# Optimization experiments

Measured on AMD Instinct MI355X. Metric: run time of the kernel, lower is better.

The kernel has to match this reference:

```python
import jax, jax.numpy as jnp
import numpy as np

FORWARD_WEIGHT = 1.0  # ChamferLoss(forward_weight=1.0)


def _chamfer_dists(pred, gt):
    """Bidirectional squared NN distances.
    pred: (B,N,3), gt: (B,M,3) -> dist1 (B,N), dist2 (B,M).
    Uses ||x-y||^2 = ||x||^2 + ||y||^2 - 2<x,y> to avoid the (B,N,M,3) diff tensor.
    """
    xx = jnp.sum(pred * pred, axis=-1)                 # (B,N)
    yy = jnp.sum(gt * gt, axis=-1)                     # (B,M)
    xy = jnp.einsum('bnd,bmd->bnm', pred, gt)          # (B,N,M)
    d = xx[:, :, None] + yy[:, None, :] - 2.0 * xy     # (B,N,M) squared distances
    dist1 = jnp.min(d, axis=2)                         # pred -> gt, (B,N)
    dist2 = jnp.min(d, axis=1)                         # gt -> pred, (B,M)
    return dist1, dist2


def setup_inputs() -> dict:
    key = jax.random.key(0)
    k1, k2 = jax.random.split(key)
    B, N, M = 4, 8192, 8192
    pred = jax.random.normal(k1, (B, N, 3), dtype=jnp.float32)
    gt = jax.random.normal(k2, (B, M, 3), dtype=jnp.float32)
    return {"pred": pred, "gt": gt}


def reference(pred, gt):
    # ChamferLoss.forward with defaults: no threshold, no masks, percentage=1.0,
    # forward_weight=1.0, reduction='mean'.
    dist1, dist2 = _chamfer_dists(pred, gt)
    pred2gt = jnp.mean(dist1, axis=1)                  # (B,)
    gt2pred = jnp.mean(dist2, axis=1)                  # (B,)
    cd_dist = FORWARD_WEIGHT * pred2gt + gt2pred
    return jnp.mean(cd_dist)
```

## Files before the change

kernel.cpp:

```cpp
#include <hip/hip_runtime.h>

typedef short short8 __attribute__((ext_vector_type(8)));
typedef float floatx16 __attribute__((ext_vector_type(16)));

#define B_    4
#define NPTS  8192
#define IS    16
#define JS    16
#define ITB   512
#define JTB   512
#define NT    4
#define NJT   16
#define TOT   (B_ * NPTS)

#define A0OFF 0
#define A1OFF 516
#define B0OFF 1032
#define B1OFF 1548
#define LDS8N 2060


__device__ __forceinline__ unsigned short bf16h(float v) {
  unsigned u = __float_as_uint(v);
  return (unsigned short)((u + 0x7FFFu + ((u >> 16) & 1u)) >> 16);
}
__device__ __forceinline__ void bf16split(float v, unsigned short& h, unsigned short& l) {
  h = bf16h(v);
  l = bf16h(v - __uint_as_float((unsigned)h << 16));
}

__device__ __forceinline__ void pack_dst(const float* g, short8& s0, short8& s1) {
  const float x = g[0], y = g[1], z = g[2];
  const float w = fmaf(x, x, fmaf(y, y, z * z));
  unsigned short xh, xl, yh, yl, zh, zl, wh, wl;
  bf16split(-2.f * x, xh, xl); bf16split(-2.f * y, yh, yl);
  bf16split(-2.f * z, zh, zl); bf16split(w, wh, wl);
  s0 = (short8){(short)xh,(short)xh,(short)xl,(short)xl,
                (short)yh,(short)yh,(short)yl,(short)yl};
  s1 = (short8){(short)zh,(short)zh,(short)zl,(short)zl,
                (short)wh,(short)wl,(short)0x3F80,(short)0x3F80};
}
__device__ __forceinline__ void pack_src(const float* p, short8& s0, short8& s1) {
  const float x = p[0], y = p[1], z = p[2];
  const float qq = fmaf(x, x, fmaf(y, y, z * z));
  unsigned short xh, xl, yh, yl, zh, zl, qh, ql;
  bf16split(x, xh, xl); bf16split(y, yh, yl);
  bf16split(z, zh, zl); bf16split(qq, qh, ql);
  s0 = (short8){(short)xh,(short)xl,(short)xh,(short)xl,
                (short)yh,(short)yl,(short)yh,(short)yl};
  s1 = (short8){(short)zh,(short)zl,(short)zh,(short)zl,
                (short)0x3F80,(short)0x3F80,(short)qh,(short)ql};
}

__global__ __launch_bounds__(256, 4) void mfma_pass_kernel(
    const float* __restrict__ pred, const float* __restrict__ gt,
    unsigned* __restrict__ slots) {
  __shared__ short8 lds8[LDS8N];

  const int zb  = blockIdx.z;
  const int dir = zb >> 2;
  const int b   = zb & 3;
  const float* src = dir ? gt   : pred;
  const float* dst = dir ? pred : gt;

  const int tid   = threadIdx.x;
  const int lane  = tid & 63;
  const int w     = tid >> 6;
  const int jbase = blockIdx.y * JTB;
  const int ibase = blockIdx.x * ITB;

#pragma unroll
  for (int r = 0; r < 2; ++r) {
    const int pt = tid + r * 256;
    short8 s0, s1;
    pack_dst(dst + ((size_t)b * NPTS + jbase + pt) * 3, s0, s1);
    lds8[A0OFF + pt] = s0;
    lds8[A1OFF + pt] = s1;
    pack_src(src + ((size_t)b * NPTS + ibase + pt) * 3, s0, s1);
    lds8[B0OFF + pt] = s0;
    lds8[B1OFF + pt] = s1;
  }
  __syncthreads();

  const int n = lane & 31;
  const int h = lane >> 5;

  short8 bf[NT];
  float  ma[NT], mb[NT];
  const int bbase = (h ? B1OFF : B0OFF) + w * 128 + n;
#pragma unroll
  for (int t = 0; t < NT; ++t) {
    bf[t] = lds8[bbase + t * 32];
    ma[t] = 1e30f;
    mb[t] = 1e30f;
  }

  const int abase = (h ? A1OFF : A0OFF) + n;
  const floatx16 zero16 = {0.f,0.f,0.f,0.f, 0.f,0.f,0.f,0.f,
                           0.f,0.f,0.f,0.f, 0.f,0.f,0.f,0.f};

  for (int jt = 0; jt < NJT; ++jt) {
    const short8 af = lds8[abase + jt * 32];
#pragma unroll
    for (int t = 0; t < NT; ++t) {
      floatx16 d = __builtin_amdgcn_mfma_f32_32x32x16_bf16(af, bf[t], zero16, 0, 0, 0);
      float ca = fminf(fminf(d[0], d[1]), d[2]);
      ca = fminf(fminf(ca, d[3]), d[4]);
      ca = fminf(fminf(ca, d[5]), d[6]);
      ma[t] = fminf(fminf(ca, d[7]), ma[t]);
      float cb = fminf(fminf(d[8], d[9]), d[10]);
      cb = fminf(fminf(cb, d[11]), d[12]);
      cb = fminf(fminf(cb, d[13]), d[14]);
      mb[t] = fminf(fminf(cb, d[15]), mb[t]);
    }
  }

#pragma unroll
  for (int t = 0; t < NT; ++t) {
    float v = fminf(ma[t], mb[t]);
    v = fminf(v, __shfl_xor(v, 32));
    if (lane < 32) {
      const int gi = ibase + w * 128 + t * 32 + lane;
      const int bi = __float_as_int(v);
      const unsigned u = (unsigned)bi ^ (unsigned)((bi >> 31) | 0x80000000);
      atomicMin(&slots[(size_t)(dir * B_ + b) * NPTS + gi], u);
    }
  }
}

__global__ __launch_bounds__(256) void pass2_kernel(
    const unsigned* __restrict__ slots, float* __restrict__ out) {
  const int gid = blockIdx.x * 256 + threadIdx.x;
  float s = 0.f;
#pragma unroll
  for (int k = 0; k < 8; ++k) {
    const unsigned u = slots[gid + k * 8192];
    const int bi = (u & 0x80000000u) ? (int)(u ^ 0x80000000u) : (int)~u;
    s += __int_as_float(bi);
  }
  __shared__ float red[256];
  const int tid = threadIdx.x;
  red[tid] = s;
  __syncthreads();
  for (int st = 128; st > 0; st >>= 1) {
    if (tid < st) red[tid] += red[tid + st];
    __syncthreads();
  }
  if (tid == 0) atomicAdd(out, red[0] * (1.0f / TOT));
}

extern "C" void kernel_launch(void* const* d_in, const int* in_sizes, int n_in,
                              void* d_out, int out_size, void* d_ws, size_t ws_size,
                              hipStream_t stream) {
  const float* pred = (const float*)d_in[0];
  const float* gt   = (const float*)d_in[1];
  unsigned* slots = (unsigned*)d_ws;
  float* out = (float*)d_out;

  hipMemsetAsync(slots, 0xFF, (size_t)2 * TOT * sizeof(unsigned), stream);
  hipMemsetAsync(out, 0, out_size * sizeof(float), stream);

  dim3 g(IS, JS, 2 * B_);
  mfma_pass_kernel<<<g, 256, 0, stream>>>(pred, gt, slots);

  pass2_kernel<<<(2 * TOT) / (256 * 8), 256, 0, stream>>>(slots, out);
}
```

Before: 76.31 us.

## Prepack bf16 operands once and give each block the full j range

A separate pack kernel converts both clouds into split-bf16 MFMA operands in global memory once, rather than having every tile block repack its own slices. The main kernel now gives each block 128 source points and the full 8192-point destination range, staged through LDS in 1024-point chunks with register prefetch of the next chunk. Because each block sees every destination point, the per-point minimum is final inside the block. This removes the atomicMin slot array, its memset and the second reduction pass in favour of a shuffle reduction plus one atomicAdd per block. The cost is fewer blocks (64x8), one accumulator tile per wave with less ILP, and two extra barriers per chunk.

Result: slower. 88.14 us (+15.5%).

```diff
diff --git a/kernel.cpp b/kernel.cpp
--- a/kernel.cpp
+++ b/kernel.cpp
@@ -5,19 +5,13 @@
 
 #define B_    4
 #define NPTS  8192
-#define IS    16
-#define JS    16
-#define ITB   512
-#define JTB   512
-#define NT    4
-#define NJT   16
+#define ITB   128
+#define ISPL  (NPTS / ITB)
+#define JCH   1024
+#define NCH   (NPTS / JCH)
+#define NJT   (JCH / 32)
 #define TOT   (B_ * NPTS)
-
-#define A0OFF 0
-#define A1OFF 516
-#define B0OFF 1032
-#define B1OFF 1548
-#define LDS8N 2060
+#define ARR   32768
 
 
 __device__ __forceinline__ unsigned short bf16h(float v) {
@@ -52,101 +46,103 @@
                 (short)0x3F80,(short)0x3F80,(short)qh,(short)ql};
 }
 
-__global__ __launch_bounds__(256, 4) void mfma_pass_kernel(
+__global__ __launch_bounds__(256) void pack_kernel(
     const float* __restrict__ pred, const float* __restrict__ gt,
-    unsigned* __restrict__ slots) {
-  __shared__ short8 lds8[LDS8N];
+    short8* __restrict__ W) {
+  const int gid = blockIdx.x * 256 + threadIdx.x;
+  const int cloud = gid >> 15;
+  const int idx = gid & (ARR - 1);
+  const float* p = (cloud ? gt : pred) + (size_t)idx * 3;
+  short8 d0, d1, s0, s1;
+  pack_dst(p, d0, d1);
+  pack_src(p, s0, s1);
+  if (cloud) {
+    W[0 * ARR + idx] = d0;  W[1 * ARR + idx] = d1;
+    W[6 * ARR + idx] = s0;  W[7 * ARR + idx] = s1;
+  } else {
+    W[2 * ARR + idx] = d0;  W[3 * ARR + idx] = d1;
+    W[4 * ARR + idx] = s0;  W[5 * ARR + idx] = s1;
+  }
+}
 
-  const int zb  = blockIdx.z;
+__global__ __launch_bounds__(256, 2) void chamfer_main(
+    const short8* __restrict__ W, float* __restrict__ out) {
+  __shared__ short8 ldsA[2 * JCH];
+  __shared__ short8 ldsB[256];
+  __shared__ float wsum[4];
+
+  const int zb  = blockIdx.y;
   const int dir = zb >> 2;
   const int b   = zb & 3;
-  const float* src = dir ? gt   : pred;
-  const float* dst = dir ? pred : gt;
+  const int tid  = threadIdx.x;
+  const int lane = tid & 63;
+  const int w    = tid >> 6;
+  const int ibase = blockIdx.x * ITB;
+  const size_t boff = (size_t)b * NPTS;
 
-  const int tid   = threadIdx.x;
-  const int lane  = tid & 63;
-  const int w     = tid >> 6;
-  const int jbase = blockIdx.y * JTB;
-  const int ibase = blockIdx.x * ITB;
+  const short8* A0 = W + (size_t)(dir ? 2 : 0) * ARR + boff;
+  const short8* A1 = W + (size_t)(dir ? 3 : 1) * ARR + boff;
+  const short8* S0 = W + (size_t)(dir ? 6 : 4) * ARR + boff;
+  const short8* S1 = W + (size_t)(dir ? 7 : 5) * ARR + boff;
 
+  ldsB[tid] = (tid < 128) ? S0[ibase + tid] : S1[ibase + tid - 128];
+
+  short8 pre[8];
 #pragma unroll
-  for (int r = 0; r < 2; ++r) {
-    const int pt = tid + r * 256;
-    short8 s0, s1;
-    pack_dst(dst + ((size_t)b * NPTS + jbase + pt) * 3, s0, s1);
-    lds8[A0OFF + pt] = s0;
-    lds8[A1OFF + pt] = s1;
-    pack_src(src + ((size_t)b * NPTS + ibase + pt) * 3, s0, s1);
-    lds8[B0OFF + pt] = s0;
-    lds8[B1OFF + pt] = s1;
+  for (int k = 0; k < 8; ++k) {
+    const int g = tid + k * 256;
+    pre[k] = (g < JCH) ? A0[g] : A1[g - JCH];
   }
+
   __syncthreads();
-
   const int n = lane & 31;
   const int h = lane >> 5;
+  const short8 bf = ldsB[h * 128 + w * 32 + n];
+  const int abase = h * JCH + n;
 
-  short8 bf[NT];
-  float  ma[NT], mb[NT];
-  const int bbase = (h ? B1OFF : B0OFF) + w * 128 + n;
-#pragma unroll
-  for (int t = 0; t < NT; ++t) {
-    bf[t] = lds8[bbase + t * 32];
-    ma[t] = 1e30f;
-    mb[t] = 1e30f;
-  }
-
-  const int abase = (h ? A1OFF : A0OFF) + n;
+  float ma = 1e30f, mb = 1e30f;
   const floatx16 zero16 = {0.f,0.f,0.f,0.f, 0.f,0.f,0.f,0.f,
                            0.f,0.f,0.f,0.f, 0.f,0.f,0.f,0.f};
 
-  for (int jt = 0; jt < NJT; ++jt) {
-    const short8 af = lds8[abase + jt * 32];
+  for (int c = 0; c < NCH; ++c) {
+    __syncthreads();
 #pragma unroll
-    for (int t = 0; t < NT; ++t) {
-      floatx16 d = __builtin_amdgcn_mfma_f32_32x32x16_bf16(af, bf[t], zero16, 0, 0, 0);
+    for (int k = 0; k < 8; ++k) ldsA[tid + k * 256] = pre[k];
+    __syncthreads();
+    if (c + 1 < NCH) {
+      const size_t cb = (size_t)(c + 1) * JCH;
+#pragma unroll
+      for (int k = 0; k < 8; ++k) {
+        const int g = tid + k * 256;
+        pre[k] = (g < JCH) ? A0[cb + g] : A1[cb + g - JCH];
+      }
+    }
+#pragma unroll 8
+    for (int jt = 0; jt < NJT; ++jt) {
+      const short8 af = ldsA[abase + jt * 32];
+      floatx16 d = __builtin_amdgcn_mfma_f32_32x32x16_bf16(af, bf, zero16, 0, 0, 0);
       float ca = fminf(fminf(d[0], d[1]), d[2]);
       ca = fminf(fminf(ca, d[3]), d[4]);
       ca = fminf(fminf(ca, d[5]), d[6]);
-      ma[t] = fminf(fminf(ca, d[7]), ma[t]);
-      float cb = fminf(fminf(d[8], d[9]), d[10]);
-      cb = fminf(fminf(cb, d[11]), d[12]);
-      cb = fminf(fminf(cb, d[13]), d[14]);
-      mb[t] = fminf(fminf(cb, d[15]), mb[t]);
+      ma = fminf(fminf(ca, d[7]), ma);
+      float cb2 = fminf(fminf(d[8], d[9]), d[10]);
+      cb2 = fminf(fminf(cb2, d[11]), d[12]);
+      cb2 = fminf(fminf(cb2, d[13]), d[14]);
+      mb = fminf(fminf(cb2, d[15]), mb);
     }
   }
 
-#pragma unroll
-  for (int t = 0; t < NT; ++t) {
-    float v = fminf(ma[t], mb[t]);
-    v = fminf(v, __shfl_xor(v, 32));
-    if (lane < 32) {
-      const int gi = ibase + w * 128 + t * 32 + lane;
-      const int bi = __float_as_int(v);
-      const unsigned u = (unsigned)bi ^ (unsigned)((bi >> 31) | 0x80000000);
-      atomicMin(&slots[(size_t)(dir * B_ + b) * NPTS + gi], u);
-    }
-  }
-}
-
-__global__ __launch_bounds__(256) void pass2_kernel(
-    const unsigned* __restrict__ slots, float* __restrict__ out) {
-  const int gid = blockIdx.x * 256 + threadIdx.x;
-  float s = 0.f;
-#pragma unroll
-  for (int k = 0; k < 8; ++k) {
-    const unsigned u = slots[gid + k * 8192];
-    const int bi = (u & 0x80000000u) ? (int)(u ^ 0x80000000u) : (int)~u;
-    s += __int_as_float(bi);
-  }
-  __shared__ float red[256];
-  const int tid = threadIdx.x;
-  red[tid] = s;
+  const float m = fminf(ma, mb);
+  float v = fminf(m, __shfl_xor(m, 32));
+  v += __shfl_xor(v, 1);
+  v += __shfl_xor(v, 2);
+  v += __shfl_xor(v, 4);
+  v += __shfl_xor(v, 8);
+  v += __shfl_xor(v, 16);
+  if (lane == 0) wsum[w] = v;
   __syncthreads();
-  for (int st = 128; st > 0; st >>= 1) {
-    if (tid < st) red[tid] += red[tid + st];
-    __syncthreads();
-  }
-  if (tid == 0) atomicAdd(out, red[0] * (1.0f / TOT));
+  if (tid == 0)
+    atomicAdd(out, (wsum[0] + wsum[1] + wsum[2] + wsum[3]) * (1.0f / TOT));
 }
 
 extern "C" void kernel_launch(void* const* d_in, const int* in_sizes, int n_in,
@@ -154,14 +150,10 @@
                               hipStream_t stream) {
   const float* pred = (const float*)d_in[0];
   const float* gt   = (const float*)d_in[1];
-  unsigned* slots = (unsigned*)d_ws;
+  short8* W  = (short8*)d_ws;
   float* out = (float*)d_out;
 
-  hipMemsetAsync(slots, 0xFF, (size_t)2 * TOT * sizeof(unsigned), stream);
   hipMemsetAsync(out, 0, out_size * sizeof(float), stream);
-
-  dim3 g(IS, JS, 2 * B_);
-  mfma_pass_kernel<<<g, 256, 0, stream>>>(pred, gt, slots);
-
-  pass2_kernel<<<(2 * TOT) / (256 * 8), 256, 0, stream>>>(slots, out);
+  pack_kernel<<<(2 * ARR) / 256, 256, 0, stream>>>(pred, gt, W);
+  chamfer_main<<<dim3(ISPL, 2 * B_), 256, 0, stream>>>(W, out);
 }
```

## Precompute bf16-split point packs once in a pre-pass kernel and drop LDS staging

Applied to the files above, without the earlier changes.

Adds a pack kernel that converts each point once into its bf16 hi/lo split fragments for both the source and destination roles, writes them to workspace, and also initializes the slots and the output, replacing the two memsets. The MFMA kernel then reads its fragments straight from global memory instead of packing into LDS behind a barrier, and its inner loop is unrolled by four. This removes the per-block repacking that was repeated across 16 tiles per point, along with the LDS traffic and the sync. In exchange it adds a kernel launch and global/L2 reads of the packed data.

After: 76.47 us. No clear change (+0.2%).

```diff
diff --git a/kernel.cpp b/kernel.cpp
--- a/kernel.cpp
+++ b/kernel.cpp
@@ -12,12 +12,7 @@
 #define NT    4
 #define NJT   16
 #define TOT   (B_ * NPTS)
-
-#define A0OFF 0
-#define A1OFF 516
-#define B0OFF 1032
-#define B1OFF 1548
-#define LDS8N 2060
+#define ARR   32768
 
 
 __device__ __forceinline__ unsigned short bf16h(float v) {
@@ -52,55 +47,59 @@
                 (short)0x3F80,(short)0x3F80,(short)qh,(short)ql};
 }
 
+__global__ __launch_bounds__(256) void pack_kernel(
+    const float* __restrict__ pred, const float* __restrict__ gt,
+    short8* __restrict__ W, unsigned* __restrict__ slots,
+    float* __restrict__ out) {
+  const int gid = blockIdx.x * 256 + threadIdx.x;
+  slots[gid] = 0xFFFFFFFFu;
+  if (gid == 0) out[0] = 0.f;
+  const int cloud = gid >> 15;
+  const int idx = gid & (ARR - 1);
+  const float* p = (cloud ? gt : pred) + (size_t)idx * 3;
+  short8 d0, d1, s0, s1;
+  pack_dst(p, d0, d1);
+  pack_src(p, s0, s1);
+  if (cloud) {
+    W[0 * ARR + idx] = d0;  W[1 * ARR + idx] = d1;
+    W[6 * ARR + idx] = s0;  W[7 * ARR + idx] = s1;
+  } else {
+    W[2 * ARR + idx] = d0;  W[3 * ARR + idx] = d1;
+    W[4 * ARR + idx] = s0;  W[5 * ARR + idx] = s1;
+  }
+}
+
 __global__ __launch_bounds__(256, 4) void mfma_pass_kernel(
-    const float* __restrict__ pred, const float* __restrict__ gt,
-    unsigned* __restrict__ slots) {
-  __shared__ short8 lds8[LDS8N];
-
+    const short8* __restrict__ W, unsigned* __restrict__ slots) {
   const int zb  = blockIdx.z;
   const int dir = zb >> 2;
   const int b   = zb & 3;
-  const float* src = dir ? gt   : pred;
-  const float* dst = dir ? pred : gt;
-
   const int tid   = threadIdx.x;
   const int lane  = tid & 63;
   const int w     = tid >> 6;
+  const int n     = lane & 31;
+  const int h     = lane >> 5;
   const int jbase = blockIdx.y * JTB;
   const int ibase = blockIdx.x * ITB;
 
-#pragma unroll
-  for (int r = 0; r < 2; ++r) {
-    const int pt = tid + r * 256;
-    short8 s0, s1;
-    pack_dst(dst + ((size_t)b * NPTS + jbase + pt) * 3, s0, s1);
-    lds8[A0OFF + pt] = s0;
-    lds8[A1OFF + pt] = s1;
-    pack_src(src + ((size_t)b * NPTS + ibase + pt) * 3, s0, s1);
-    lds8[B0OFF + pt] = s0;
-    lds8[B1OFF + pt] = s1;
-  }
-  __syncthreads();
-
-  const int n = lane & 31;
-  const int h = lane >> 5;
+  const short8* Ap = W + (size_t)(dir * 2 + h) * ARR + (size_t)b * NPTS + jbase;
+  const short8* Bp = W + (size_t)(4 + dir * 2 + h) * ARR + (size_t)b * NPTS + ibase;
 
   short8 bf[NT];
   float  ma[NT], mb[NT];
-  const int bbase = (h ? B1OFF : B0OFF) + w * 128 + n;
 #pragma unroll
   for (int t = 0; t < NT; ++t) {
-    bf[t] = lds8[bbase + t * 32];
+    bf[t] = Bp[w * 128 + t * 32 + n];
     ma[t] = 1e30f;
     mb[t] = 1e30f;
   }
 
-  const int abase = (h ? A1OFF : A0OFF) + n;
   const floatx16 zero16 = {0.f,0.f,0.f,0.f, 0.f,0.f,0.f,0.f,
                            0.f,0.f,0.f,0.f, 0.f,0.f,0.f,0.f};
 
+#pragma unroll 4
   for (int jt = 0; jt < NJT; ++jt) {
-    const short8 af = lds8[abase + jt * 32];
+    const short8 af = Ap[jt * 32 + n];
 #pragma unroll
     for (int t = 0; t < NT; ++t) {
       floatx16 d = __builtin_amdgcn_mfma_f32_32x32x16_bf16(af, bf[t], zero16, 0, 0, 0);
@@ -154,14 +153,11 @@
                               hipStream_t stream) {
   const float* pred = (const float*)d_in[0];
   const float* gt   = (const float*)d_in[1];
-  unsigned* slots = (unsigned*)d_ws;
+  short8* W = (short8*)d_ws;
+  unsigned* slots = (unsigned*)(W + 8 * ARR);
   float* out = (float*)d_out;
 
-  hipMemsetAsync(slots, 0xFF, (size_t)2 * TOT * sizeof(unsigned), stream);
-  hipMemsetAsync(out, 0, out_size * sizeof(float), stream);
-
-  dim3 g(IS, JS, 2 * B_);
-  mfma_pass_kernel<<<g, 256, 0, stream>>>(pred, gt, slots);
-
+  pack_kernel<<<(2 * ARR) / 256, 256, 0, stream>>>(pred, gt, W, slots, out);
+  mfma_pass_kernel<<<dim3(IS, JS, 2 * B_), 256, 0, stream>>>(W, slots);
   pass2_kernel<<<(2 * TOT) / (256 * 8), 256, 0, stream>>>(slots, out);
 }
```
